# Performance work log

Hardware: AMD Instinct MI355X
Metric: run time of the kernel (lower is better)

The kernel has to match this reference:

```python
import jax, jax.numpy as jnp
import numpy as np

DIM = 96
HEADS = 6
WS = 8                      # window_size
OWS = int(WS * 0.5) + WS    # overlap_win_size = 12
PAD = (OWS - WS) // 2       # 2
Dd = Hh = Ww = 24
B = 1
L = Dd * Hh * Ww
MLP_H = DIM * 2
TBL = (WS + OWS - 1) ** 3   # 6859 relative-position-bias entries


def setup_inputs() -> dict:
    key = jax.random.key(0)
    ks = jax.random.split(key, 8)
    def n(k, shape, s=0.02):
        return jax.random.normal(k, shape, jnp.float32) * s
    return {
        "x": jax.random.normal(ks[0], (B, L, DIM), jnp.float32),
        "ln1_w": jnp.ones((DIM,), jnp.float32),
        "ln1_b": jnp.zeros((DIM,), jnp.float32),
        "qkv_w": n(ks[1], (3 * DIM, DIM)),
        "qkv_b": jnp.zeros((3 * DIM,), jnp.float32),
        "rpb": n(ks[2], (TBL, HEADS)),
        "proj_w": n(ks[3], (DIM, DIM)),
        "proj_b": jnp.zeros((DIM,), jnp.float32),
        "ln2_w": jnp.ones((DIM,), jnp.float32),
        "ln2_b": jnp.zeros((DIM,), jnp.float32),
        "fc1_w": n(ks[4], (MLP_H, DIM)),
        "fc1_b": jnp.zeros((MLP_H,), jnp.float32),
        "fc2_w": n(ks[5], (DIM, MLP_H)),
        "fc2_b": jnp.zeros((DIM,), jnp.float32),
        "rpi": jax.random.randint(ks[6], (WS ** 3, OWS ** 3), 0, TBL),
        "D": Dd, "H": Hh, "W": Ww,
    }


def _ln(x, w, b):
    m = jnp.mean(x, -1, keepdims=True)
    v = jnp.var(x, -1, keepdims=True)
    return (x - m) / jnp.sqrt(v + 1e-5) * w + b


def _ocab3d(x, ln1_w, ln1_b, qkv_w, qkv_b, rpb, proj_w, proj_b,
            ln2_w, ln2_b, fc1_w, fc1_b, fc2_w, fc2_b, rpi, D, H, W):
    Bz, Lz, C = x.shape
    hd = C // HEADS
    scale = hd ** -0.5
    shortcut = x

    xn = _ln(x, ln1_w, ln1_b).reshape(Bz, D, H, W, C)
    qkv = xn @ qkv_w.T + qkv_b                   # [B,D,H,W,3C]
    q = qkv[..., :C]
    kv = qkv[..., C:]                            # cat(k, v) on channels, [B,D,H,W,2C]

    nD, nH, nW = D // WS, H // WS, W // WS
    nw = nD * nH * nW

    # non-overlapping query windows -> [B*nw, WS^3, C]
    qw = q.reshape(Bz, nD, WS, nH, WS, nW, WS, C)
    qw = qw.transpose(0, 1, 3, 5, 2, 4, 6, 7).reshape(Bz * nw, WS ** 3, C)

    # overlapping kv windows via pad + strided gather (mirrors F.pad + unfold)
    kvp = jnp.pad(kv, ((0, 0), (PAD, PAD), (PAD, PAD), (PAD, PAD), (0, 0)))
    idx_d = (jnp.arange(nD) * WS)[:, None] + jnp.arange(OWS)[None, :]
    idx_h = (jnp.arange(nH) * WS)[:, None] + jnp.arange(OWS)[None, :]
    idx_w = (jnp.arange(nW) * WS)[:, None] + jnp.arange(OWS)[None, :]
    kw = kvp[:, idx_d]                 # [B,nD,OWS,Hp,Wp,2C]
    kw = kw[:, :, :, idx_h]            # [B,nD,OWS,nH,OWS,Wp,2C]
    kw = kw[:, :, :, :, :, idx_w]      # [B,nD,OWS,nH,OWS,nW,OWS,2C]
    kw = kw.transpose(0, 1, 3, 5, 2, 4, 6, 7).reshape(Bz * nw, OWS ** 3, 2 * C)
    kk, vv = kw[..., :C], kw[..., C:]

    qh = qw.reshape(-1, WS ** 3, HEADS, hd).transpose(0, 2, 1, 3) * scale
    kh = kk.reshape(-1, OWS ** 3, HEADS, hd).transpose(0, 2, 1, 3)
    vh = vv.reshape(-1, OWS ** 3, HEADS, hd).transpose(0, 2, 1, 3)

    attn = jnp.einsum('bhqd,bhkd->bhqk', qh, kh)               # [B*nw,H,512,1728]
    bias = rpb[rpi.reshape(-1)].reshape(WS ** 3, OWS ** 3, HEADS).transpose(2, 0, 1)
    attn = jax.nn.softmax(attn + bias[None], axis=-1)
    out = jnp.einsum('bhqk,bhkd->bhqd', attn, vh)
    out = out.transpose(0, 2, 1, 3).reshape(Bz * nw, WS ** 3, C)

    # window reverse -> [B, L, C]
    out = out.reshape(Bz, nD, nH, nW, WS, WS, WS, C)
    out = out.transpose(0, 1, 4, 2, 5, 3, 6, 7).reshape(Bz, D * H * W, C)

    x2 = out @ proj_w.T + proj_b + shortcut
    h1 = jax.nn.gelu(_ln(x2, ln2_w, ln2_b) @ fc1_w.T + fc1_b, approximate=False)
    return x2 + (h1 @ fc2_w.T + fc2_b)


def reference(x, ln1_w, ln1_b, qkv_w, qkv_b, rpb, proj_w, proj_b,
              ln2_w, ln2_b, fc1_w, fc1_b, fc2_w, fc2_b, rpi, D, H, W):
    return _ocab3d(x, ln1_w, ln1_b, qkv_w, qkv_b, rpb, proj_w, proj_b,
                   ln2_w, ln2_b, fc1_w, fc1_b, fc2_w, fc2_b, rpi, D, H, W)
```

## Files before the change

kernel.cpp:

```cpp
#include <hip/hip_runtime.h>
#include <math.h>

#define DIMC   96
#define NHEADS 6
#define HD     16
#define WSZ    8
#define OWSZ   12
#define PADW   2
#define DD     24
#define LTOK   13824
#define NWIN   27
#define NKEY   1728
#define NROW   512
#define MLPH   192
#define PDIM   28
#define PD3    21952
#define TBL    6859
#define LSTR   82944
#define AOSTR  1327104

typedef __attribute__((ext_vector_type(4))) short bf16x4;
typedef __attribute__((ext_vector_type(8))) short bf16x8;
typedef __attribute__((ext_vector_type(4))) float f32x4;

__device__ __forceinline__ unsigned short bfround(float f) {
    unsigned u = __float_as_uint(f);
    return (unsigned short)((u + 0x7FFFu + ((u >> 16) & 1u)) >> 16);
}
__device__ __forceinline__ unsigned bfpack(float a, float b) {
    unsigned ua = __float_as_uint(a), ub = __float_as_uint(b);
    ua = (ua + 0x7FFFu + ((ua >> 16) & 1u)) >> 16;
    ub = (ub + 0x7FFFu + ((ub >> 16) & 1u)) >> 16;
    return ua | (ub << 16);
}
__device__ __forceinline__ uint4 pack8(const float* v) {
    uint4 u;
    u.x = bfpack(v[0], v[1]); u.y = bfpack(v[2], v[3]);
    u.z = bfpack(v[4], v[5]); u.w = bfpack(v[6], v[7]);
    return u;
}
__device__ __forceinline__ bf16x4 pack4(f32x4 p) {
    union { uint2 u; bf16x4 v; } r;
    r.u.x = __builtin_amdgcn_perm(__float_as_uint(p[1]), __float_as_uint(p[0]), 0x07060302u);
    r.u.y = __builtin_amdgcn_perm(__float_as_uint(p[3]), __float_as_uint(p[2]), 0x07060302u);
    return r.v;
}
__device__ __forceinline__ f32x4 mfma16(bf16x4 a, bf16x4 b, f32x4 c) {
#if __has_builtin(__builtin_amdgcn_mfma_f32_16x16x16bf16_1k)
    return __builtin_amdgcn_mfma_f32_16x16x16bf16_1k(a, b, c, 0, 0, 0);
#else
    bf16x8 a8 = {a[0], a[1], a[2], a[3], 0, 0, 0, 0};
    bf16x8 b8 = {b[0], b[1], b[2], b[3], 0, 0, 0, 0};
    return __builtin_amdgcn_mfma_f32_16x16x32_bf16(a8, b8, c, 0, 0, 0);
#endif
}

#define PREQ  2592
#define NZB   515
__global__ __launch_bounds__(256) void pre_kernel(
        const float* __restrict__ X, const float* __restrict__ W,
        const float* __restrict__ bias, const float* __restrict__ lnw,
        const float* __restrict__ lnb,
        const int* __restrict__ rpi, const float* __restrict__ rpb,
        unsigned short* __restrict__ q16, unsigned short* __restrict__ kvp2,
        float* __restrict__ biasP) {
    __shared__ uint4 Af4[2 * 3 * 4 * 16];
    __shared__ uint4 Bf4[6 * 3 * 4 * 16];
    int bx = blockIdx.x, tid = threadIdx.x;

    if (bx >= PREQ) {
        int t = (bx - PREQ) * 256 + tid;
        if (t < 21952 * 6) {
            int head = t / PD3, pos = t % PD3;
            int d = pos / 784, h = (pos / 28) % 28, w = pos % 28;
            if (d < 2 || d >= 26 || h < 2 || h >= 26 || w < 2 || w >= 26) {
                uint4* p = (uint4*)(kvp2 + ((long)head * PD3 + pos) * 32);
                uint4 z = make_uint4(0, 0, 0, 0);
                p[0] = z; p[1] = z; p[2] = z; p[3] = z;
            }
        }
        return;
    }

    if (bx & 1) {
        int b2 = bx >> 1;
        int head = b2 / 216;
        int r2 = b2 % 216;
        int kt = r2 >> 1, qh = r2 & 1;
        int k0 = kt * 16;
        int qi = qh * 256 + tid;
        const int* rp = rpi + (long)qi * NKEY + k0;
        int idx[16];
        #pragma unroll
        for (int j = 0; j < 4; ++j) {
            int4 t = *(const int4*)(rp + j * 4);
            idx[j*4+0] = t.x; idx[j*4+1] = t.y; idx[j*4+2] = t.z; idx[j*4+3] = t.w;
        }
        #pragma unroll
        for (int quad = 0; quad < 4; ++quad) {
            float4 v;
            v.x = rpb[idx[quad*4+0] * NHEADS + head];
            v.y = rpb[idx[quad*4+1] * NHEADS + head];
            v.z = rpb[idx[quad*4+2] * NHEADS + head];
            v.w = rpb[idx[quad*4+3] * NHEADS + head];
            *(float4*)(biasP + ((((long)head*108 + kt)*4 + quad)*512 + qi)*4) = v;
        }
        return;
    }

    int b2 = bx >> 1;
    int nc   = b2 % 3;
    int row0 = (b2 / 3) * 32;

    if (tid < 128) {
        int row = tid >> 2, part = tid & 3;
        int rt = row >> 4, mm = row & 15;
        float v[24];
        const float4* xp = (const float4*)(X + (long)(row0 + row) * 96 + part * 24);
        float s = 0.f, sq = 0.f;
        #pragma unroll
        for (int i = 0; i < 6; ++i) {
            float4 t = xp[i];
            v[i*4+0] = t.x; v[i*4+1] = t.y; v[i*4+2] = t.z; v[i*4+3] = t.w;
            s  += t.x + t.y + t.z + t.w;
            sq += t.x*t.x + t.y*t.y + t.z*t.z + t.w*t.w;
        }
        s  += __shfl_xor(s, 1);  s  += __shfl_xor(s, 2);
        sq += __shfl_xor(sq, 1); sq += __shfl_xor(sq, 2);
        float mean = s * (1.f / 96.f);
        float inv  = rsqrtf(sq * (1.f / 96.f) - mean * mean + 1e-5f);
        const float4* wp = (const float4*)(lnw + part * 24);
        const float4* bp = (const float4*)(lnb + part * 24);
        #pragma unroll
        for (int i = 0; i < 6; ++i) {
            float4 wv = wp[i], bv = bp[i];
            v[i*4+0] = (v[i*4+0] - mean) * inv * wv.x + bv.x;
            v[i*4+1] = (v[i*4+1] - mean) * inv * wv.y + bv.y;
            v[i*4+2] = (v[i*4+2] - mean) * inv * wv.z + bv.z;
            v[i*4+3] = (v[i*4+3] - mean) * inv * wv.w + bv.w;
        }
        #pragma unroll
        for (int gg = 0; gg < 3; ++gg) {
            int g = part * 3 + gg;
            int kt = g >> 2, qq = g & 3;
            Af4[((rt * 3 + kt) * 4 + qq) * 16 + mm] = pack8(v + gg * 8);
        }
    }
    for (int idx = tid; idx < 96 * 12; idx += 256) {
        int n = idx / 12;
        int g = idx % 12;
        const float4* wp = (const float4*)(W + (long)(nc * 96 + n) * 96 + g * 8);
        float v[8];
        float4 t0 = wp[0], t1 = wp[1];
        v[0]=t0.x; v[1]=t0.y; v[2]=t0.z; v[3]=t0.w;
        v[4]=t1.x; v[5]=t1.y; v[6]=t1.z; v[7]=t1.w;
        int ct = n >> 4, nn = n & 15, kt = g >> 2, qg = g & 3;
        Bf4[((ct * 3 + kt) * 4 + qg) * 16 + nn] = pack8(v);
    }
    __syncthreads();

    int wave = tid >> 6, lane = tid & 63;
    int qq = lane >> 4, mI = lane & 15;
    int rt = wave & 1, cg = wave >> 1;

    f32x4 acc[3];
    #pragma unroll
    for (int j = 0; j < 3; ++j) acc[j] = (f32x4){0.f, 0.f, 0.f, 0.f};
    #pragma unroll
    for (int kt = 0; kt < 3; ++kt) {
        bf16x8 a = *(const bf16x8*)&Af4[((rt * 3 + kt) * 4 + qq) * 16 + mI];
        #pragma unroll
        for (int j = 0; j < 3; ++j) {
            bf16x8 b = *(const bf16x8*)&Bf4[(((cg * 3 + j) * 3 + kt) * 4 + qq) * 16 + mI];
            acc[j] = __builtin_amdgcn_mfma_f32_16x16x32_bf16(a, b, acc[j], 0, 0, 0);
        }
    }

    float bv[3];
    #pragma unroll
    for (int j = 0; j < 3; ++j) bv[j] = bias[nc * 96 + (cg * 3 + j) * 16 + mI];
    #pragma unroll
    for (int r = 0; r < 4; ++r) {
        int row = row0 + rt * 16 + qq * 4 + r;
        if (nc == 0) {
            unsigned short* op = q16 + (long)row * 96;
            #pragma unroll
            for (int j = 0; j < 3; ++j)
                op[(cg * 3 + j) * 16 + mI] = bfround(0.25f * (acc[j][r] + bv[j]));
        } else {
            int d = row / 576, hh = (row / 24) % 24, w2 = row % 24;
            long pos = ((long)(d + 2) * 28 + (hh + 2)) * 28 + (w2 + 2);
            #pragma unroll
            for (int j = 0; j < 3; ++j) {
                int head = cg * 3 + j;
                kvp2[((long)head * PD3 + pos) * 32 +
                     (nc == 2 ? 16 : 0) + mI] = bfround(acc[j][r] + bv[j]);
            }
        }
    }
}

#define KSTR 20
#define VSTR 68
__global__ __launch_bounds__(256) void attn_kernel(
        const unsigned short* __restrict__ q, const unsigned short* __restrict__ kvp2,
        const float* __restrict__ biasP, float* __restrict__ ao,
        float* __restrict__ lbuf) {
    __shared__ unsigned short Ks[2][64 * KSTR];
    __shared__ unsigned short Vs[2][16 * VSTR];
    int bid = blockIdx.x;
    int w = bid / 48, rem = bid % 48;
    int head = rem >> 3;
    int quart = (rem >> 1) & 3, half = rem & 1;
    int wd8 = (w / 9) * 8, wh8 = ((w / 3) % 3) * 8, ww8 = (w % 3) * 8;
    int tid = threadIdx.x, wave = tid >> 6, lane = tid & 63;
    int quad = lane >> 4, m16 = lane & 15;
    int key = tid >> 2, part = tid & 3;
    int c0 = half ? 13 : 0;
    int cn = half ? 14 : 13;

    auto kvaddr = [&](int c) -> const uint4* {
        int jg = c * 64 + key;
        int i = jg / 144, jh = (jg / 12) % 12, jw = jg % 12;
        long sp = ((long)(wd8 + i) * PDIM + (wh8 + jh)) * PDIM + (ww8 + jw);
        return (const uint4*)(kvp2 + ((long)head * PD3 + sp) * 32 + part * 8);
    };
    auto writeLDS = [&](int b, uint4 v) {
        if (part < 2) {
            *(uint2*)(&Ks[b][key * KSTR + part * 8])     = make_uint2(v.x, v.y);
            *(uint2*)(&Ks[b][key * KSTR + part * 8 + 4]) = make_uint2(v.z, v.w);
        } else {
            int d0 = (part - 2) * 8;
            Vs[b][(d0+0)*VSTR + key] = (unsigned short)(v.x);
            Vs[b][(d0+1)*VSTR + key] = (unsigned short)(v.x >> 16);
            Vs[b][(d0+2)*VSTR + key] = (unsigned short)(v.y);
            Vs[b][(d0+3)*VSTR + key] = (unsigned short)(v.y >> 16);
            Vs[b][(d0+4)*VSTR + key] = (unsigned short)(v.z);
            Vs[b][(d0+5)*VSTR + key] = (unsigned short)(v.z >> 16);
            Vs[b][(d0+6)*VSTR + key] = (unsigned short)(v.w);
            Vs[b][(d0+7)*VSTR + key] = (unsigned short)(v.w >> 16);
        }
    };

    int grow[2]; bf16x4 qf[2];
    #pragma unroll
    for (int qt = 0; qt < 2; ++qt) {
        int ql = quart * 128 + wave * 32 + qt * 16 + m16;
        int ld = ql >> 6, lh = (ql >> 3) & 7, lw = ql & 7;
        grow[qt] = ((wd8 + ld) * 24 + (wh8 + lh)) * 24 + (ww8 + lw);
        qf[qt] = *(const bf16x4*)(q + (long)grow[qt] * 96 + head * 16 + quad * 4);
    }

    const float* bbase = biasP + (long)head * 884736 + quad * 2048
                         + ((quart * 128 + wave * 32 + m16) << 2);
    f32x4 bcur[2][4];
    #pragma unroll
    for (int qt = 0; qt < 2; ++qt)
        #pragma unroll
        for (int kt = 0; kt < 4; ++kt)
            bcur[qt][kt] = *(const f32x4*)(bbase + (long)(c0*4 + kt) * 8192 + qt * 64);

    writeLDS(0, *kvaddr(c0));

    f32x4 o[2];
    o[0] = (f32x4){0.f,0.f,0.f,0.f}; o[1] = (f32x4){0.f,0.f,0.f,0.f};
    float l[2] = {0.f, 0.f};
    uint4 stgn;

    #pragma unroll 1
    for (int cc = 0; cc < cn; ++cc) {
        int c = c0 + cc;
        if (cc + 1 < cn) stgn = *kvaddr(c + 1);
        __syncthreads();
        int b = cc & 1;

        bf16x4 kf[4];
        #pragma unroll
        for (int kt = 0; kt < 4; ++kt)
            kf[kt] = *(const bf16x4*)(&Ks[b][(kt * 16 + m16) * KSTR + quad * 4]);

        f32x4 S[2][4];
        #pragma unroll
        for (int qt = 0; qt < 2; ++qt)
            #pragma unroll
            for (int kt = 0; kt < 4; ++kt)
                S[qt][kt] = mfma16(kf[kt], qf[qt], bcur[qt][kt]);

        f32x4 bnxt[2][4];
        if (cc + 1 < cn) {
            const float* bp = bbase + (long)(c + 1) * 32768;
            #pragma unroll
            for (int qt = 0; qt < 2; ++qt)
                #pragma unroll
                for (int kt = 0; kt < 4; ++kt)
                    bnxt[qt][kt] = *(const f32x4*)(bp + kt * 8192 + qt * 64);
        }

        #pragma unroll
        for (int qt = 0; qt < 2; ++qt) {
            float ls = 0.f;
            #pragma unroll
            for (int kt = 0; kt < 4; ++kt)
                #pragma unroll
                for (int r = 0; r < 4; ++r) {
                    float p = __expf(S[qt][kt][r]);
                    S[qt][kt][r] = p; ls += p;
                }
            l[qt] += ls;
        }

        #pragma unroll
        for (int kt = 0; kt < 4; ++kt) {
            bf16x4 vf = *(const bf16x4*)(&Vs[b][m16 * VSTR + kt * 16 + quad * 4]);
            o[0] = mfma16(vf, pack4(S[0][kt]), o[0]);
            o[1] = mfma16(vf, pack4(S[1][kt]), o[1]);
        }

        if (cc + 1 < cn) writeLDS((cc + 1) & 1, stgn);
        #pragma unroll
        for (int qt = 0; qt < 2; ++qt)
            #pragma unroll
            for (int kt = 0; kt < 4; ++kt) bcur[qt][kt] = bnxt[qt][kt];
    }

    float* aout = ao + (long)half * AOSTR;
    float* lout = lbuf + (long)half * LSTR;
    #pragma unroll
    for (int qt = 0; qt < 2; ++qt) {
        float lq = l[qt];
        lq += __shfl_xor(lq, 16);
        lq += __shfl_xor(lq, 32);
        float4* op = (float4*)(aout + (long)grow[qt] * 96 + head * 16 + quad * 4);
        *op = make_float4(o[qt][0], o[qt][1], o[qt][2], o[qt][3]);
        if (quad == 0) lout[grow[qt] * 6 + head] = lq;
    }
}

__global__ __launch_bounds__(256) void mlp_kernel(
        const float* __restrict__ ao0, const float* __restrict__ ao1,
        const float* __restrict__ lbuf,
        const float* __restrict__ projw, const float* __restrict__ projb,
        const float* __restrict__ x,
        const float* __restrict__ ln2w, const float* __restrict__ ln2b,
        const float* __restrict__ fc1w, const float* __restrict__ fc1b,
        const float* __restrict__ fc2w, const float* __restrict__ fc2b,
        float* __restrict__ out) {
    __shared__ uint4 Af4[2 * 3 * 4 * 16];
    __shared__ uint4 Bf4[6 * 3 * 4 * 16];
    __shared__ float x2s[32 * 96];
    __shared__ unsigned short h16[32 * 192];
    int tid = threadIdx.x;
    int row0 = blockIdx.x * 32;
    int wave = tid >> 6, lane = tid & 63;
    int qq = lane >> 4, mI = lane & 15;
    int rt = wave & 1, cg = wave >> 1;

    if (tid < 128) {
        int row = tid >> 2, part = tid & 3;
        int rtA = row >> 4, mm = row & 15;
        int grow = row0 + row;
        const float4* a0 = (const float4*)(ao0 + (long)grow * 96 + part * 24);
        const float4* a1 = (const float4*)(ao1 + (long)grow * 96 + part * 24);
        int ha = (part * 3) >> 1, hb = ha + 1;
        float inva = 1.f / (lbuf[grow*6 + ha] + lbuf[LSTR + grow*6 + ha]);
        float invb = 1.f / (lbuf[grow*6 + hb] + lbuf[LSTR + grow*6 + hb]);
        float v[24];
        #pragma unroll
        for (int i = 0; i < 6; ++i) {
            float4 u0 = a0[i], u1 = a1[i];
            #pragma unroll
            for (int j = 0; j < 4; ++j) {
                int gc = part * 24 + i * 4 + j;
                float lv = ((gc >> 4) == ha) ? inva : invb;
                float s = (j==0?u0.x+u1.x : j==1?u0.y+u1.y : j==2?u0.z+u1.z : u0.w+u1.w);
                v[i*4+j] = s * lv;
            }
        }
        #pragma unroll
        for (int gg = 0; gg < 3; ++gg) {
            int g = part * 3 + gg;
            int kt = g >> 2, q4 = g & 3;
            Af4[((rtA * 3 + kt) * 4 + q4) * 16 + mm] = pack8(v + gg * 8);
        }
    }
    for (int idx = tid; idx < 96 * 12; idx += 256) {
        int n = idx / 12, g = idx % 12;
        const float4* wp = (const float4*)(projw + (long)n * 96 + g * 8);
        float v[8];
        float4 t0 = wp[0], t1 = wp[1];
        v[0]=t0.x; v[1]=t0.y; v[2]=t0.z; v[3]=t0.w;
        v[4]=t1.x; v[5]=t1.y; v[6]=t1.z; v[7]=t1.w;
        int ct = n >> 4, nn = n & 15, kt = g >> 2, qg = g & 3;
        Bf4[((ct * 3 + kt) * 4 + qg) * 16 + nn] = pack8(v);
    }
    __syncthreads();

    {
        f32x4 acc[3];
        #pragma unroll
        for (int j = 0; j < 3; ++j) acc[j] = (f32x4){0.f,0.f,0.f,0.f};
        #pragma unroll
        for (int kt = 0; kt < 3; ++kt) {
            bf16x8 a = *(const bf16x8*)&Af4[((rt * 3 + kt) * 4 + qq) * 16 + mI];
            #pragma unroll
            for (int j = 0; j < 3; ++j) {
                bf16x8 b = *(const bf16x8*)&Bf4[(((cg * 3 + j) * 3 + kt) * 4 + qq) * 16 + mI];
                acc[j] = __builtin_amdgcn_mfma_f32_16x16x32_bf16(a, b, acc[j], 0, 0, 0);
            }
        }
        float bv[3];
        #pragma unroll
        for (int j = 0; j < 3; ++j) bv[j] = projb[(cg * 3 + j) * 16 + mI];
        #pragma unroll
        for (int r = 0; r < 4; ++r) {
            int row = rt * 16 + qq * 4 + r;
            int grow = row0 + row;
            #pragma unroll
            for (int j = 0; j < 3; ++j) {
                int col = (cg * 3 + j) * 16 + mI;
                x2s[row * 96 + col] = acc[j][r] + bv[j] + x[(long)grow * 96 + col];
            }
        }
    }
    __syncthreads();

    if (tid < 128) {
        int row = tid >> 2, part = tid & 3;
        int rtA = row >> 4, mm = row & 15;
        float v[24];
        const float4* xp = (const float4*)(x2s + row * 96 + part * 24);
        float s = 0.f, sq = 0.f;
        #pragma unroll
        for (int i = 0; i < 6; ++i) {
            float4 t = xp[i];
            v[i*4+0] = t.x; v[i*4+1] = t.y; v[i*4+2] = t.z; v[i*4+3] = t.w;
            s  += t.x + t.y + t.z + t.w;
            sq += t.x*t.x + t.y*t.y + t.z*t.z + t.w*t.w;
        }
        s  += __shfl_xor(s, 1);  s  += __shfl_xor(s, 2);
        sq += __shfl_xor(sq, 1); sq += __shfl_xor(sq, 2);
        float mean = s * (1.f / 96.f);
        float inv  = rsqrtf(sq * (1.f / 96.f) - mean * mean + 1e-5f);
        const float4* wp = (const float4*)(ln2w + part * 24);
        const float4* bp = (const float4*)(ln2b + part * 24);
        #pragma unroll
        for (int i = 0; i < 6; ++i) {
            float4 wv = wp[i], bv = bp[i];
            v[i*4+0] = (v[i*4+0] - mean) * inv * wv.x + bv.x;
            v[i*4+1] = (v[i*4+1] - mean) * inv * wv.y + bv.y;
            v[i*4+2] = (v[i*4+2] - mean) * inv * wv.z + bv.z;
            v[i*4+3] = (v[i*4+3] - mean) * inv * wv.w + bv.w;
        }
        #pragma unroll
        for (int gg = 0; gg < 3; ++gg) {
            int g = part * 3 + gg;
            int kt = g >> 2, q4 = g & 3;
            Af4[((rtA * 3 + kt) * 4 + q4) * 16 + mm] = pack8(v + gg * 8);
        }
    }

    #pragma unroll 1
    for (int nc = 0; nc < 2; ++nc) {
        if (nc) __syncthreads();
        for (int idx = tid; idx < 96 * 12; idx += 256) {
            int n = idx / 12, g = idx % 12;
            const float4* wp = (const float4*)(fc1w + (long)(nc * 96 + n) * 96 + g * 8);
            float v[8];
            float4 t0 = wp[0], t1 = wp[1];
            v[0]=t0.x; v[1]=t0.y; v[2]=t0.z; v[3]=t0.w;
            v[4]=t1.x; v[5]=t1.y; v[6]=t1.z; v[7]=t1.w;
            int ct = n >> 4, nn = n & 15, kt = g >> 2, qg = g & 3;
            Bf4[((ct * 3 + kt) * 4 + qg) * 16 + nn] = pack8(v);
        }
        __syncthreads();

        f32x4 acc[3];
        #pragma unroll
        for (int j = 0; j < 3; ++j) acc[j] = (f32x4){0.f,0.f,0.f,0.f};
        #pragma unroll
        for (int kt = 0; kt < 3; ++kt) {
            bf16x8 a = *(const bf16x8*)&Af4[((rt * 3 + kt) * 4 + qq) * 16 + mI];
            #pragma unroll
            for (int j = 0; j < 3; ++j) {
                bf16x8 b = *(const bf16x8*)&Bf4[(((cg * 3 + j) * 3 + kt) * 4 + qq) * 16 + mI];
                acc[j] = __builtin_amdgcn_mfma_f32_16x16x32_bf16(a, b, acc[j], 0, 0, 0);
            }
        }
        float bv[3];
        #pragma unroll
        for (int j = 0; j < 3; ++j) bv[j] = fc1b[nc * 96 + (cg * 3 + j) * 16 + mI];
        #pragma unroll
        for (int r = 0; r < 4; ++r) {
            int row = rt * 16 + qq * 4 + r;
            #pragma unroll
            for (int j = 0; j < 3; ++j) {
                int col = nc * 96 + (cg * 3 + j) * 16 + mI;
                float v = acc[j][r] + bv[j];
                float g = 0.5f * v * (1.f + erff(v * 0.70710678f));
                int fi = (((row >> 4) * 6 + (col >> 5)) * 4 + ((col >> 3) & 3)) * 16 + (row & 15);
                h16[fi * 8 + (col & 7)] = bfround(g);
            }
        }
    }

    f32x4 acc2[3];
    #pragma unroll
    for (int j = 0; j < 3; ++j) acc2[j] = (f32x4){0.f,0.f,0.f,0.f};
    #pragma unroll 1
    for (int kh = 0; kh < 2; ++kh) {
        __syncthreads();
        for (int idx = tid; idx < 96 * 12; idx += 256) {
            int n = idx / 12, g = idx % 12;
            const float4* wp = (const float4*)(fc2w + (long)n * 192 + kh * 96 + g * 8);
            float v[8];
            float4 t0 = wp[0], t1 = wp[1];
            v[0]=t0.x; v[1]=t0.y; v[2]=t0.z; v[3]=t0.w;
            v[4]=t1.x; v[5]=t1.y; v[6]=t1.z; v[7]=t1.w;
            int ct = n >> 4, nn = n & 15, kt = g >> 2, qg = g & 3;
            Bf4[((ct * 3 + kt) * 4 + qg) * 16 + nn] = pack8(v);
        }
        __syncthreads();
        #pragma unroll
        for (int kt = 0; kt < 3; ++kt) {
            int ktA = kh * 3 + kt;
            bf16x8 a = *(const bf16x8*)&h16[(((rt * 6 + ktA) * 4 + qq) * 16 + mI) * 8];
            #pragma unroll
            for (int j = 0; j < 3; ++j) {
                bf16x8 b = *(const bf16x8*)&Bf4[(((cg * 3 + j) * 3 + kt) * 4 + qq) * 16 + mI];
                acc2[j] = __builtin_amdgcn_mfma_f32_16x16x32_bf16(a, b, acc2[j], 0, 0, 0);
            }
        }
    }
    float bv[3];
    #pragma unroll
    for (int j = 0; j < 3; ++j) bv[j] = fc2b[(cg * 3 + j) * 16 + mI];
    #pragma unroll
    for (int r = 0; r < 4; ++r) {
        int row = rt * 16 + qq * 4 + r;
        int grow = row0 + row;
        #pragma unroll
        for (int j = 0; j < 3; ++j) {
            int col = (cg * 3 + j) * 16 + mI;
            out[(long)grow * 96 + col] = acc2[j][r] + bv[j] + x2s[row * 96 + col];
        }
    }
}

extern "C" void kernel_launch(void* const* d_in, const int* in_sizes, int n_in,
                              void* d_out, int out_size, void* d_ws, size_t ws_size,
                              hipStream_t stream) {
    const float* x     = (const float*)d_in[0];
    const float* ln1w  = (const float*)d_in[1];
    const float* ln1b  = (const float*)d_in[2];
    const float* qkvw  = (const float*)d_in[3];
    const float* qkvb  = (const float*)d_in[4];
    const float* rpb   = (const float*)d_in[5];
    const float* projw = (const float*)d_in[6];
    const float* projb = (const float*)d_in[7];
    const float* ln2w  = (const float*)d_in[8];
    const float* ln2b  = (const float*)d_in[9];
    const float* fc1w  = (const float*)d_in[10];
    const float* fc1b  = (const float*)d_in[11];
    const float* fc2w  = (const float*)d_in[12];
    const float* fc2b  = (const float*)d_in[13];
    const int*   rpi   = (const int*)d_in[14];
    float* outp = (float*)d_out;

    float* ws = (float*)d_ws;
    float*          aop    = ws;
    unsigned short* q16    = (unsigned short*)(ws + 2654208);
    unsigned short* kvp16  = (unsigned short*)(ws + 3317760);
    float*          biasPf = ws + 5425152;
    float*          lbuf   = ws + 10733568;

    pre_kernel<<<PREQ + NZB, 256, 0, stream>>>(x, qkvw, qkvb, ln1w, ln1b,
                                               rpi, rpb, q16, kvp16, biasPf);
    attn_kernel<<<NWIN * NHEADS * 4 * 2, 256, 0, stream>>>(q16, kvp16, biasPf, aop, lbuf);
    mlp_kernel<<<432, 256, 0, stream>>>(aop, aop + AOSTR, lbuf, projw, projb, x,
                                        ln2w, ln2b, fc1w, fc1b, fc2w, fc2b, outp);
}
```

Before: 196.2 us.

## Prepack MLP weights once to bf16 and split bias gather into its own kernel

```diff
diff --git a/kernel.cpp b/kernel.cpp
--- a/kernel.cpp
+++ b/kernel.cpp
@@ -55,21 +55,43 @@
 #endif
 }
 
-#define PREQ  2592
-#define NZB   515
-__global__ __launch_bounds__(256) void pre_kernel(
+#define QKVB 1296
+#define ZB   515
+#define WPB  45
+__global__ __launch_bounds__(256) void qkvz_kernel(
         const float* __restrict__ X, const float* __restrict__ W,
         const float* __restrict__ bias, const float* __restrict__ lnw,
         const float* __restrict__ lnb,
-        const int* __restrict__ rpi, const float* __restrict__ rpb,
+        const float* __restrict__ projw, const float* __restrict__ fc1w,
+        const float* __restrict__ fc2w,
         unsigned short* __restrict__ q16, unsigned short* __restrict__ kvp2,
-        float* __restrict__ biasP) {
+        uint4* __restrict__ wpack) {
     __shared__ uint4 Af4[2 * 3 * 4 * 16];
     __shared__ uint4 Bf4[6 * 3 * 4 * 16];
     int bx = blockIdx.x, tid = threadIdx.x;
 
-    if (bx >= PREQ) {
-        int t = (bx - PREQ) * 256 + tid;
+    if (bx >= QKVB + ZB) {
+        int u = (bx - QKVB - ZB) * 256 + tid;
+        if (u < 5760) {
+            int p = (u < 1152) ? u : (u < 3456 ? (u - 1152) % 1152 : (u - 3456) % 1152);
+            int nn = p & 15, r = p >> 4, qg = r & 3, r2 = r >> 2;
+            int kt = r2 % 3, ct = r2 / 3;
+            int n = ct * 16 + nn, g = kt * 4 + qg;
+            const float* src;
+            if (u < 1152)      src = projw + n * 96 + g * 8;
+            else if (u < 3456) { int nc = (u - 1152) / 1152; src = fc1w + (long)(nc * 96 + n) * 96 + g * 8; }
+            else               { int kh = (u - 3456) / 1152; src = fc2w + (long)n * 192 + kh * 96 + g * 8; }
+            const float4* s4 = (const float4*)src;
+            float v[8];
+            float4 t0 = s4[0], t1 = s4[1];
+            v[0]=t0.x; v[1]=t0.y; v[2]=t0.z; v[3]=t0.w;
+            v[4]=t1.x; v[5]=t1.y; v[6]=t1.z; v[7]=t1.w;
+            wpack[u] = pack8(v);
+        }
+        return;
+    }
+    if (bx >= QKVB) {
+        int t = (bx - QKVB) * 256 + tid;
         if (t < 21952 * 6) {
             int head = t / PD3, pos = t % PD3;
             int d = pos / 784, h = (pos / 28) % 28, w = pos % 28;
@@ -82,35 +104,8 @@
         return;
     }
 
-    if (bx & 1) {
-        int b2 = bx >> 1;
-        int head = b2 / 216;
-        int r2 = b2 % 216;
-        int kt = r2 >> 1, qh = r2 & 1;
-        int k0 = kt * 16;
-        int qi = qh * 256 + tid;
-        const int* rp = rpi + (long)qi * NKEY + k0;
-        int idx[16];
-        #pragma unroll
-        for (int j = 0; j < 4; ++j) {
-            int4 t = *(const int4*)(rp + j * 4);
-            idx[j*4+0] = t.x; idx[j*4+1] = t.y; idx[j*4+2] = t.z; idx[j*4+3] = t.w;
-        }
-        #pragma unroll
-        for (int quad = 0; quad < 4; ++quad) {
-            float4 v;
-            v.x = rpb[idx[quad*4+0] * NHEADS + head];
-            v.y = rpb[idx[quad*4+1] * NHEADS + head];
-            v.z = rpb[idx[quad*4+2] * NHEADS + head];
-            v.w = rpb[idx[quad*4+3] * NHEADS + head];
-            *(float4*)(biasP + ((((long)head*108 + kt)*4 + quad)*512 + qi)*4) = v;
-        }
-        return;
-    }
-
-    int b2 = bx >> 1;
-    int nc   = b2 % 3;
-    int row0 = (b2 / 3) * 32;
+    int nc   = bx % 3;
+    int row0 = (bx / 3) * 32;
 
     if (tid < 128) {
         int row = tid >> 2, part = tid & 3;
@@ -197,6 +192,33 @@
                      (nc == 2 ? 16 : 0) + mI] = bfround(acc[j][r] + bv[j]);
             }
         }
+    }
+}
+
+__global__ __launch_bounds__(256) void bias_kernel(
+        const int* __restrict__ rpi, const float* __restrict__ rpb,
+        float* __restrict__ biasP) {
+    int bx = blockIdx.x;
+    int head = bx / 216;
+    int r2 = bx % 216;
+    int kt = r2 >> 1, qh = r2 & 1;
+    int k0 = kt * 16;
+    int qi = qh * 256 + threadIdx.x;
+    const int* rp = rpi + (long)qi * NKEY + k0;
+    int idx[16];
+    #pragma unroll
+    for (int j = 0; j < 4; ++j) {
+        int4 t = *(const int4*)(rp + j * 4);
+        idx[j*4+0] = t.x; idx[j*4+1] = t.y; idx[j*4+2] = t.z; idx[j*4+3] = t.w;
+    }
+    #pragma unroll
+    for (int quad = 0; quad < 4; ++quad) {
+        float4 v;
+        v.x = rpb[idx[quad*4+0] * NHEADS + head];
+        v.y = rpb[idx[quad*4+1] * NHEADS + head];
+        v.z = rpb[idx[quad*4+2] * NHEADS + head];
+        v.w = rpb[idx[quad*4+3] * NHEADS + head];
+        *(float4*)(biasP + ((((long)head*108 + kt)*4 + quad)*512 + qi)*4) = v;
     }
 }
 
@@ -338,15 +360,13 @@
 
 __global__ __launch_bounds__(256) void mlp_kernel(
         const float* __restrict__ ao0, const float* __restrict__ ao1,
-        const float* __restrict__ lbuf,
-        const float* __restrict__ projw, const float* __restrict__ projb,
-        const float* __restrict__ x,
+        const float* __restrict__ lbuf, const uint4* __restrict__ wpack,
+        const float* __restrict__ projb, const float* __restrict__ x,
         const float* __restrict__ ln2w, const float* __restrict__ ln2b,
-        const float* __restrict__ fc1w, const float* __restrict__ fc1b,
-        const float* __restrict__ fc2w, const float* __restrict__ fc2b,
+        const float* __restrict__ fc1b, const float* __restrict__ fc2b,
         float* __restrict__ out) {
+    __shared__ uint4 Ws[5760];
     __shared__ uint4 Af4[2 * 3 * 4 * 16];
-    __shared__ uint4 Bf4[6 * 3 * 4 * 16];
     __shared__ float x2s[32 * 96];
     __shared__ unsigned short h16[32 * 192];
     int tid = threadIdx.x;
@@ -354,6 +374,8 @@
     int wave = tid >> 6, lane = tid & 63;
     int qq = lane >> 4, mI = lane & 15;
     int rt = wave & 1, cg = wave >> 1;
+
+    for (int idx = tid; idx < 5760; idx += 256) Ws[idx] = wpack[idx];
 
     if (tid < 128) {
         int row = tid >> 2, part = tid & 3;
@@ -383,16 +405,6 @@
             Af4[((rtA * 3 + kt) * 4 + q4) * 16 + mm] = pack8(v + gg * 8);
         }
     }
-    for (int idx = tid; idx < 96 * 12; idx += 256) {
-        int n = idx / 12, g = idx % 12;
-        const float4* wp = (const float4*)(projw + (long)n * 96 + g * 8);
-        float v[8];
-        float4 t0 = wp[0], t1 = wp[1];
-        v[0]=t0.x; v[1]=t0.y; v[2]=t0.z; v[3]=t0.w;
-        v[4]=t1.x; v[5]=t1.y; v[6]=t1.z; v[7]=t1.w;
-        int ct = n >> 4, nn = n & 15, kt = g >> 2, qg = g & 3;
-        Bf4[((ct * 3 + kt) * 4 + qg) * 16 + nn] = pack8(v);
-    }
     __syncthreads();
 
     {
@@ -404,7 +416,7 @@
             bf16x8 a = *(const bf16x8*)&Af4[((rt * 3 + kt) * 4 + qq) * 16 + mI];
             #pragma unroll
             for (int j = 0; j < 3; ++j) {
-                bf16x8 b = *(const bf16x8*)&Bf4[(((cg * 3 + j) * 3 + kt) * 4 + qq) * 16 + mI];
+                bf16x8 b = *(const bf16x8*)&Ws[(((cg * 3 + j) * 3 + kt) * 4 + qq) * 16 + mI];
                 acc[j] = __builtin_amdgcn_mfma_f32_16x16x32_bf16(a, b, acc[j], 0, 0, 0);
             }
         }
@@ -458,22 +470,10 @@
             Af4[((rtA * 3 + kt) * 4 + q4) * 16 + mm] = pack8(v + gg * 8);
         }
     }
-
-    #pragma unroll 1
+    __syncthreads();
+
+    #pragma unroll
     for (int nc = 0; nc < 2; ++nc) {
-        if (nc) __syncthreads();
-        for (int idx = tid; idx < 96 * 12; idx += 256) {
-            int n = idx / 12, g = idx % 12;
-            const float4* wp = (const float4*)(fc1w + (long)(nc * 96 + n) * 96 + g * 8);
-            float v[8];
-            float4 t0 = wp[0], t1 = wp[1];
-            v[0]=t0.x; v[1]=t0.y; v[2]=t0.z; v[3]=t0.w;
-            v[4]=t1.x; v[5]=t1.y; v[6]=t1.z; v[7]=t1.w;
-            int ct = n >> 4, nn = n & 15, kt = g >> 2, qg = g & 3;
-            Bf4[((ct * 3 + kt) * 4 + qg) * 16 + nn] = pack8(v);
-        }
-        __syncthreads();
-
         f32x4 acc[3];
         #pragma unroll
         for (int j = 0; j < 3; ++j) acc[j] = (f32x4){0.f,0.f,0.f,0.f};
@@ -482,7 +482,8 @@
             bf16x8 a = *(const bf16x8*)&Af4[((rt * 3 + kt) * 4 + qq) * 16 + mI];
             #pragma unroll
             for (int j = 0; j < 3; ++j) {
-                bf16x8 b = *(const bf16x8*)&Bf4[(((cg * 3 + j) * 3 + kt) * 4 + qq) * 16 + mI];
+                bf16x8 b = *(const bf16x8*)&Ws[1152 + nc * 1152 +
+                               (((cg * 3 + j) * 3 + kt) * 4 + qq) * 16 + mI];
                 acc[j] = __builtin_amdgcn_mfma_f32_16x16x32_bf16(a, b, acc[j], 0, 0, 0);
             }
         }
@@ -502,31 +503,21 @@
             }
         }
     }
+    __syncthreads();
 
     f32x4 acc2[3];
     #pragma unroll
     for (int j = 0; j < 3; ++j) acc2[j] = (f32x4){0.f,0.f,0.f,0.f};
-    #pragma unroll 1
+    #pragma unroll
     for (int kh = 0; kh < 2; ++kh) {
-        __syncthreads();
-        for (int idx = tid; idx < 96 * 12; idx += 256) {
-            int n = idx / 12, g = idx % 12;
-            const float4* wp = (const float4*)(fc2w + (long)n * 192 + kh * 96 + g * 8);
-            float v[8];
-            float4 t0 = wp[0], t1 = wp[1];
-            v[0]=t0.x; v[1]=t0.y; v[2]=t0.z; v[3]=t0.w;
-            v[4]=t1.x; v[5]=t1.y; v[6]=t1.z; v[7]=t1.w;
-            int ct = n >> 4, nn = n & 15, kt = g >> 2, qg = g & 3;
-            Bf4[((ct * 3 + kt) * 4 + qg) * 16 + nn] = pack8(v);
-        }
-        __syncthreads();
         #pragma unroll
         for (int kt = 0; kt < 3; ++kt) {
             int ktA = kh * 3 + kt;
             bf16x8 a = *(const bf16x8*)&h16[(((rt * 6 + ktA) * 4 + qq) * 16 + mI) * 8];
             #pragma unroll
             for (int j = 0; j < 3; ++j) {
-                bf16x8 b = *(const bf16x8*)&Bf4[(((cg * 3 + j) * 3 + kt) * 4 + qq) * 16 + mI];
+                bf16x8 b = *(const bf16x8*)&Ws[3456 + kh * 1152 +
+                               (((cg * 3 + j) * 3 + kt) * 4 + qq) * 16 + mI];
                 acc2[j] = __builtin_amdgcn_mfma_f32_16x16x32_bf16(a, b, acc2[j], 0, 0, 0);
             }
         }
@@ -572,10 +563,12 @@
     unsigned short* kvp16  = (unsigned short*)(ws + 3317760);
     float*          biasPf = ws + 5425152;
     float*          lbuf   = ws + 10733568;
-
-    pre_kernel<<<PREQ + NZB, 256, 0, stream>>>(x, qkvw, qkvb, ln1w, ln1b,
-                                               rpi, rpb, q16, kvp16, biasPf);
+    uint4*          wpack  = (uint4*)(ws + 10899456);
+
+    qkvz_kernel<<<QKVB + ZB + WPB, 256, 0, stream>>>(
+        x, qkvw, qkvb, ln1w, ln1b, projw, fc1w, fc2w, q16, kvp16, wpack);
+    bias_kernel<<<1296, 256, 0, stream>>>(rpi, rpb, biasPf);
     attn_kernel<<<NWIN * NHEADS * 4 * 2, 256, 0, stream>>>(q16, kvp16, biasPf, aop, lbuf);
-    mlp_kernel<<<432, 256, 0, stream>>>(aop, aop + AOSTR, lbuf, projw, projb, x,
-                                        ln2w, ln2b, fc1w, fc1b, fc2w, fc2b, outp);
-}
+    mlp_kernel<<<432, 256, 0, stream>>>(aop, aop + AOSTR, lbuf, wpack, projb, x,
+                                        ln2w, ln2b, fc1b, fc2b, outp);
+}
```

New measurement: 193.0 us. No clear change (-1.6%).
